# Kernel tuning notes

Hardware: AMD Instinct MI355X
Metric: run time of the kernel (lower is better)

The kernel has to match this reference:

```python
import jax, jax.numpy as jnp
import numpy as np
from jax import lax

T, I, H = 8192, 1024, 1024


def setup_inputs() -> dict:
    key = jax.random.key(0)
    ks = jax.random.split(key, 7)
    s = 1.0 / np.sqrt(H)
    x = jax.random.normal(ks[0], (T, I), dtype=jnp.float32)
    W_ih = jax.random.uniform(ks[1], (4 * H, I), minval=-s, maxval=s, dtype=jnp.float32)
    W_hh = jax.random.uniform(ks[2], (4 * H, H), minval=-s, maxval=s, dtype=jnp.float32)
    b_ih = jax.random.uniform(ks[3], (4 * H,), minval=-s, maxval=s, dtype=jnp.float32)
    b_hh = jax.random.uniform(ks[4], (4 * H,), minval=-s, maxval=s, dtype=jnp.float32)
    h0 = jax.random.normal(ks[5], (H,), dtype=jnp.float32)
    c0 = jax.random.uniform(ks[6], (H,), dtype=jnp.float32)
    return {"x": x, "W_ih": W_ih, "W_hh": W_hh, "b_ih": b_ih, "b_hh": b_hh, "h0": h0, "c0": c0}


def reference(x, W_ih, W_hh, b_ih, b_hh, h0, c0):
    # Precompute the input contribution to all gates in one big GEMM: [T, 4H]
    gates_x = x @ W_ih.T + (b_ih + b_hh)

    def step(carry, gx):
        h, c = carry
        g = gx + h @ W_hh.T  # [4H]
        i, f, gc, o = jnp.split(g, 4)  # PyTorch gate order: input, forget, cell, output
        i = jax.nn.sigmoid(i)
        f = jax.nn.sigmoid(f)
        gc = jnp.tanh(gc)
        o = jax.nn.sigmoid(o)
        c_new = f * c + i * gc
        h_new = o * jnp.tanh(c_new)
        return (h_new, c_new), h_new

    (_, _), hs = lax.scan(step, (h0, c0), gates_x)
    return hs  # [T, H] — the per-timestep outputs collected in fullDataOutput
```

## Files before the change

kernel.cpp:

```cpp
#include <hip/hip_runtime.h>
#include <cstdint>

#define T_STEPS 8192
#define HDIM    1024
#define NBLK    128
#define NTHR    512

typedef unsigned int u32x4 __attribute__((ext_vector_type(4)));

__device__ __forceinline__ float dot4(float4 a, float4 b) {
    return a.x * b.x + a.y * b.y + a.z * b.z + a.w * b.w;
}
__device__ __forceinline__ float sigmoidf_(float v) { return 1.0f / (1.0f + __expf(-v)); }
__device__ __forceinline__ float tanhf_(float v)    { return 1.0f - 2.0f / (__expf(2.0f * v) + 1.0f); }

__device__ __forceinline__ u32x4 poll2(unsigned long long a) {
    u32x4 r;
    asm volatile("global_load_dwordx4 %0, %1, off sc0 sc1\n\t"
                 "s_waitcnt vmcnt(0)"
                 : "=&v"(r) : "v"(a) : "memory");
    return r;
}

__global__ __launch_bounds__(NTHR, 2)
void lstm_persistent(const float* __restrict__ x,
                     const float* __restrict__ W_ih,
                     const float* __restrict__ W_hh,
                     const float* __restrict__ b_ih,
                     const float* __restrict__ b_hh,
                     const float* __restrict__ h0,
                     const float* __restrict__ c0,
                     float* __restrict__ out,
                     unsigned long long* __restrict__ ring)
{
    __shared__ float h_lds[2][HDIM];

    const int tid = threadIdx.x;
    const int w   = tid >> 6;
    const int l   = tid & 63;
    const int u   = (blockIdx.x << 3) + w;

    float4 Whh[4][4], Wih[4][4];
#pragma unroll
    for (int q = 0; q < 4; ++q) {
        const float* rh = W_hh + (size_t)(q * HDIM + u) * HDIM;
        const float* ri = W_ih + (size_t)(q * HDIM + u) * HDIM;
#pragma unroll
        for (int i = 0; i < 4; ++i) {
            Whh[q][i] = *(const float4*)(rh + 4 * l + 256 * i);
            Wih[q][i] = *(const float4*)(ri + 4 * l + 256 * i);
        }
    }
    float bias[4];
#pragma unroll
    for (int q = 0; q < 4; ++q) bias[q] = b_ih[q * HDIM + u] + b_hh[q * HDIM + u];
    float c = c0[u];

    float4 hr[4];
#pragma unroll
    for (int i = 0; i < 4; ++i) hr[i] = *(const float4*)(h0 + 4 * l + 256 * i);

    float gxp[4];
    {
        float4 x0[4];
#pragma unroll
        for (int i = 0; i < 4; ++i) x0[i] = *(const float4*)(x + 4 * l + 256 * i);
#pragma unroll
        for (int q = 0; q < 4; ++q) {
            float a = 0.f;
#pragma unroll
            for (int i = 0; i < 4; ++i) a += dot4(Wih[q][i], x0[i]);
            gxp[q] = a;
        }
    }
    float4 xr[4], xn[4];
#pragma unroll
    for (int i = 0; i < 4; ++i) xr[i] = *(const float4*)(x + HDIM + 4 * l + 256 * i);

    for (int t = 0; t < T_STEPS; ++t) {
        float acc[4];
#pragma unroll
        for (int q = 0; q < 4; ++q) {
            float a = gxp[q];
#pragma unroll
            for (int i = 0; i < 4; ++i) a += dot4(Whh[q][i], hr[i]);
            acc[q] = a;
        }
#pragma unroll
        for (int m = 1; m < 64; m <<= 1) {
#pragma unroll
            for (int q = 0; q < 4; ++q) acc[q] += __shfl_xor(acc[q], m, 64);
        }
        const float gi = sigmoidf_(acc[0] + bias[0]);
        const float gf = sigmoidf_(acc[1] + bias[1]);
        const float gg = tanhf_   (acc[2] + bias[2]);
        const float go = sigmoidf_(acc[3] + bias[3]);
        c = gf * c + gi * gg;
        const float hval = go * tanhf_(c);

        if (l == 0) {
            const unsigned long long pk =
                ((unsigned long long)(unsigned)(t + 1) << 32) |
                (unsigned long long)__float_as_uint(hval);
            __hip_atomic_store(&ring[(t & 1) * HDIM + u], pk,
                               __ATOMIC_RELAXED, __HIP_MEMORY_SCOPE_AGENT);
            out[(size_t)t * HDIM + u] = hval;
        }
        if (t == T_STEPS - 1) break;

        {
            const int tn = (t + 2 < T_STEPS) ? (t + 2) : (T_STEPS - 1);
            const float* xp = x + (size_t)tn * HDIM;
#pragma unroll
            for (int i = 0; i < 4; ++i) xn[i] = *(const float4*)(xp + 4 * l + 256 * i);
        }
#pragma unroll
        for (int q = 0; q < 4; ++q) {
            float a = 0.f;
#pragma unroll
            for (int i = 0; i < 4; ++i) a += dot4(Wih[q][i], xr[i]);
            gxp[q] = a;
        }

        {
            const unsigned e = (unsigned)(t + 1);
            const unsigned long long base =
                (unsigned long long)(ring + (t & 1) * HDIM + 2 * tid);
            u32x4 p;
            for (;;) {
                p = poll2(base);
                if ((unsigned)p.y == e && (unsigned)p.w == e) break;
            }
            const int ns = (t + 1) & 1;
            h_lds[ns][2 * tid    ] = __uint_as_float((unsigned)p.x);
            h_lds[ns][2 * tid + 1] = __uint_as_float((unsigned)p.z);
        }
        __syncthreads();
        {
            const int ns = (t + 1) & 1;
#pragma unroll
            for (int i = 0; i < 4; ++i)
                hr[i] = *(const float4*)&h_lds[ns][4 * l + 256 * i];
        }
#pragma unroll
        for (int i = 0; i < 4; ++i) xr[i] = xn[i];
    }
}

extern "C" void kernel_launch(void* const* d_in, const int* in_sizes, int n_in,
                              void* d_out, int out_size, void* d_ws, size_t ws_size,
                              hipStream_t stream)
{
    const float* x    = (const float*)d_in[0];
    const float* W_ih = (const float*)d_in[1];
    const float* W_hh = (const float*)d_in[2];
    const float* b_ih = (const float*)d_in[3];
    const float* b_hh = (const float*)d_in[4];
    const float* h0   = (const float*)d_in[5];
    const float* c0   = (const float*)d_in[6];

    unsigned long long* ring = (unsigned long long*)d_ws;
    hipMemsetAsync(d_ws, 0, 2 * HDIM * sizeof(unsigned long long), stream);
    lstm_persistent<<<NBLK, NTHR, 0, stream>>>(x, W_ih, W_hh, b_ih, b_hh, h0, c0,
                                               (float*)d_out, ring);
}
```

Before: 25.82 ms.

## Spread LSTM units over 256 blocks of 4 waves, poll 4 ring entries per thread

New measurement: 23.40 ms. -9.4%, faster.

```diff
diff --git a/kernel.cpp b/kernel.cpp
--- a/kernel.cpp
+++ b/kernel.cpp
@@ -3,26 +3,19 @@
 
 #define T_STEPS 8192
 #define HDIM    1024
-#define NBLK    128
-#define NTHR    512
+#define NBLK    256
+#define NTHR    256
 
+typedef float        f32x4 __attribute__((ext_vector_type(4)));
 typedef unsigned int u32x4 __attribute__((ext_vector_type(4)));
 
-__device__ __forceinline__ float dot4(float4 a, float4 b) {
-    return a.x * b.x + a.y * b.y + a.z * b.z + a.w * b.w;
+__device__ __forceinline__ float dot4(f32x4 a, f32x4 b) {
+    return a[0] * b[0] + a[1] * b[1] + a[2] * b[2] + a[3] * b[3];
 }
 __device__ __forceinline__ float sigmoidf_(float v) { return 1.0f / (1.0f + __expf(-v)); }
 __device__ __forceinline__ float tanhf_(float v)    { return 1.0f - 2.0f / (__expf(2.0f * v) + 1.0f); }
 
-__device__ __forceinline__ u32x4 poll2(unsigned long long a) {
-    u32x4 r;
-    asm volatile("global_load_dwordx4 %0, %1, off sc0 sc1\n\t"
-                 "s_waitcnt vmcnt(0)"
-                 : "=&v"(r) : "v"(a) : "memory");
-    return r;
-}
-
-__global__ __launch_bounds__(NTHR, 2)
+__global__ __launch_bounds__(NTHR, 1)
 void lstm_persistent(const float* __restrict__ x,
                      const float* __restrict__ W_ih,
                      const float* __restrict__ W_hh,
@@ -38,44 +31,50 @@
     const int tid = threadIdx.x;
     const int w   = tid >> 6;
     const int l   = tid & 63;
-    const int u   = (blockIdx.x << 3) + w;
+    const int u   = (blockIdx.x << 2) + w;
 
-    float4 Whh[4][4], Wih[4][4];
+    f32x4 whh[16], wih[16];
 #pragma unroll
     for (int q = 0; q < 4; ++q) {
-        const float* rh = W_hh + (size_t)(q * HDIM + u) * HDIM;
-        const float* ri = W_ih + (size_t)(q * HDIM + u) * HDIM;
+        const float* rh = W_hh + (size_t)(q * HDIM + u) * HDIM + 4 * l;
+        const float* ri = W_ih + (size_t)(q * HDIM + u) * HDIM + 4 * l;
 #pragma unroll
         for (int i = 0; i < 4; ++i) {
-            Whh[q][i] = *(const float4*)(rh + 4 * l + 256 * i);
-            Wih[q][i] = *(const float4*)(ri + 4 * l + 256 * i);
+            whh[q * 4 + i] = *(const f32x4*)(rh + 256 * i);
+            wih[q * 4 + i] = *(const f32x4*)(ri + 256 * i);
         }
     }
+#pragma unroll
+    for (int k = 0; k < 16; ++k) {
+        asm volatile("" : "+v"(whh[k]));
+        asm volatile("" : "+v"(wih[k]));
+    }
+
     float bias[4];
 #pragma unroll
     for (int q = 0; q < 4; ++q) bias[q] = b_ih[q * HDIM + u] + b_hh[q * HDIM + u];
     float c = c0[u];
 
-    float4 hr[4];
+    f32x4 hr[4];
 #pragma unroll
-    for (int i = 0; i < 4; ++i) hr[i] = *(const float4*)(h0 + 4 * l + 256 * i);
+    for (int i = 0; i < 4; ++i) hr[i] = *(const f32x4*)(h0 + 4 * l + 256 * i);
 
     float gxp[4];
     {
-        float4 x0[4];
+        f32x4 x0[4];
 #pragma unroll
-        for (int i = 0; i < 4; ++i) x0[i] = *(const float4*)(x + 4 * l + 256 * i);
+        for (int i = 0; i < 4; ++i) x0[i] = *(const f32x4*)(x + 4 * l + 256 * i);
 #pragma unroll
         for (int q = 0; q < 4; ++q) {
             float a = 0.f;
 #pragma unroll
-            for (int i = 0; i < 4; ++i) a += dot4(Wih[q][i], x0[i]);
+            for (int i = 0; i < 4; ++i) a += dot4(wih[q * 4 + i], x0[i]);
             gxp[q] = a;
         }
     }
-    float4 xr[4], xn[4];
+    f32x4 xr[4], xn[4];
 #pragma unroll
-    for (int i = 0; i < 4; ++i) xr[i] = *(const float4*)(x + HDIM + 4 * l + 256 * i);
+    for (int i = 0; i < 4; ++i) xr[i] = *(const f32x4*)(x + HDIM + 4 * l + 256 * i);
 
     for (int t = 0; t < T_STEPS; ++t) {
         float acc[4];
@@ -83,7 +82,7 @@
         for (int q = 0; q < 4; ++q) {
             float a = gxp[q];
 #pragma unroll
-            for (int i = 0; i < 4; ++i) a += dot4(Whh[q][i], hr[i]);
+            for (int i = 0; i < 4; ++i) a += dot4(whh[q * 4 + i], hr[i]);
             acc[q] = a;
         }
 #pragma unroll
@@ -112,35 +111,45 @@
             const int tn = (t + 2 < T_STEPS) ? (t + 2) : (T_STEPS - 1);
             const float* xp = x + (size_t)tn * HDIM;
 #pragma unroll
-            for (int i = 0; i < 4; ++i) xn[i] = *(const float4*)(xp + 4 * l + 256 * i);
+            for (int i = 0; i < 4; ++i) xn[i] = *(const f32x4*)(xp + 4 * l + 256 * i);
         }
 #pragma unroll
         for (int q = 0; q < 4; ++q) {
             float a = 0.f;
 #pragma unroll
-            for (int i = 0; i < 4; ++i) a += dot4(Wih[q][i], xr[i]);
+            for (int i = 0; i < 4; ++i) a += dot4(wih[q * 4 + i], xr[i]);
             gxp[q] = a;
         }
 
         {
             const unsigned e = (unsigned)(t + 1);
             const unsigned long long base =
-                (unsigned long long)(ring + (t & 1) * HDIM + 2 * tid);
-            u32x4 p;
+                (unsigned long long)(ring + (t & 1) * HDIM + 4 * tid);
+            u32x4 p0, p1;
             for (;;) {
-                p = poll2(base);
-                if ((unsigned)p.y == e && (unsigned)p.w == e) break;
+                asm volatile(
+                    "global_load_dwordx4 %0, %2, off sc0 sc1\n\t"
+                    "global_load_dwordx4 %1, %2, off offset:16 sc0 sc1\n\t"
+                    "s_waitcnt vmcnt(0)"
+                    : "=&v"(p0), "=&v"(p1)
+                    : "v"(base)
+                    : "memory");
+                if (p0[1] == e && p0[3] == e && p1[1] == e && p1[3] == e) break;
             }
             const int ns = (t + 1) & 1;
-            h_lds[ns][2 * tid    ] = __uint_as_float((unsigned)p.x);
-            h_lds[ns][2 * tid + 1] = __uint_as_float((unsigned)p.z);
+            f32x4 hv;
+            hv[0] = __uint_as_float(p0[0]);
+            hv[1] = __uint_as_float(p0[2]);
+            hv[2] = __uint_as_float(p1[0]);
+            hv[3] = __uint_as_float(p1[2]);
+            *(f32x4*)&h_lds[ns][4 * tid] = hv;
         }
         __syncthreads();
         {
             const int ns = (t + 1) & 1;
 #pragma unroll
             for (int i = 0; i < 4; ++i)
-                hr[i] = *(const float4*)&h_lds[ns][4 * l + 256 * i];
+                hr[i] = *(const f32x4*)&h_lds[ns][4 * l + 256 * i];
         }
 #pragma unroll
         for (int i = 0; i < 4; ++i) xr[i] = xn[i];
```
